# Kernel optimization log

Hardware: AMD Instinct MI355X
Metric: run time of the kernel (lower is better)

The kernel has to match this reference:

```python
import jax, jax.numpy as jnp
import numpy as np

S = 16        # neighbor samples per layer
NL = 2        # number of GNN layers


def setup_inputs() -> dict:
    key = jax.random.key(0)
    ks = jax.random.split(key, 12)
    N_NODES, D, E, NMP, DEG, N_EDGE, B, NC = 50000, 128, 32, 3, 32, 200000, 1024, 8
    sc = 0.05
    return {
        "ids": jax.random.randint(ks[0], (B,), 0, N_NODES, dtype=jnp.int32),
        "feats": jax.random.normal(ks[1], (N_NODES, D), jnp.float32),
        "edge_emb": jax.random.normal(ks[2], (NMP, N_EDGE, E), jnp.float32),
        "adj_nodes": jax.random.randint(ks[3], (NMP, N_NODES, DEG), 0, N_NODES, dtype=jnp.int32),
        "adj_edges": jax.random.randint(ks[4], (NMP, N_NODES, DEG), 0, N_EDGE, dtype=jnp.int32),
        "W_self": jax.random.normal(ks[5], (NMP, NL, D, D), jnp.float32) * sc,
        "W_neigh": jax.random.normal(ks[6], (NMP, NL, D + E, D), jnp.float32) * sc,
        "W_edge": jax.random.normal(ks[7], (NMP, NL, 2 * D + E, E), jnp.float32) * sc,
        "attn": jax.random.normal(ks[8], (D,), jnp.float32) * sc,
        "fc_w": jax.random.normal(ks[9], (D, NC), jnp.float32) * sc,
        "fc_b": jnp.zeros((NC,), jnp.float32),
    }


def reference(ids, feats, edge_emb, adj_nodes, adj_edges, W_self, W_neigh, W_edge, attn, fc_w, fc_b):
    NMP = adj_nodes.shape[0]
    outs = []
    for mp in range(NMP):
        # --- sample neighbor tree (deterministic: first S columns) ---
        cur = ids
        all_feats = [feats[cur]]
        all_edges = []
        for _ in range(NL):
            nb = adj_nodes[mp][cur][:, :S].reshape(-1)     # [N*S]
            eid = adj_edges[mp][cur][:, :S].reshape(-1)    # [N*S]
            all_edges.append(edge_emb[mp][eid])            # [N*S, E]
            cur = nb
            all_feats.append(feats[cur])
        # --- per-layer aggregation + edge update ---
        for l in range(NL):
            new_feats = []
            for k in range(len(all_feats) - 1):
                xs, xn, ee = all_feats[k], all_feats[k + 1], all_edges[k]
                N = xs.shape[0]
                # mean over sampled neighbors of [neigh_feat || edge_emb]
                nin = jnp.concatenate(
                    [xn.reshape(N, S, -1), ee.reshape(N, S, -1)], axis=-1
                ).mean(axis=1)                             # [N, D+E]
                new_feats.append(jax.nn.relu(xs @ W_self[mp, l] + nin @ W_neigh[mp, l]))
            all_feats = new_feats  # dropout is identity in eval mode
            new_edges = []
            for k in range(len(all_edges) - 1):
                xs, xn, ee = all_feats[k], all_feats[k + 1], all_edges[k]
                rep = jnp.repeat(xs, S, axis=0)            # [N*S, D]
                new_edges.append(jax.nn.relu(
                    jnp.concatenate([rep, xn, ee], axis=-1) @ W_edge[mp, l]))
            all_edges = new_edges
        outs.append(all_feats[0])                          # [B, D]
    stacked = jnp.stack(outs)                              # [NMP, B, D]
    # metapath attention fuse
    scores = jnp.tanh(jnp.einsum('mbd,d->mb', stacked, attn))
    beta = jax.nn.softmax(scores, axis=0)
    emb = jnp.einsum('mb,mbd->bd', beta, stacked)          # [B, D]
    # F.normalize(dim=1)
    emb = emb / jnp.maximum(jnp.linalg.norm(emb, axis=1, keepdims=True), 1e-12)
    return emb @ fc_w + fc_b
```

## Files before the change

kernel.cpp:

```cpp
#include <hip/hip_runtime.h>

#define NNODES  50000
#define D       128
#define E       32
#define NMP     3
#define DEG     32
#define NEDGE   200000
#define B       1024
#define NC      8
#define S       16

#define RPM      17408
#define NKT      9
#define WSTRIDE  36864
#define WESTRIDE 9216

#define CONV_TASKS (1600000 + 6 * WSTRIDE + 3 * WESTRIDE)
#define TOT_TASKS  (CONV_TASKS + 3 * RPM)

typedef float f4 __attribute__((ext_vector_type(4)));
typedef short bh8 __attribute__((ext_vector_type(8)));
typedef unsigned int uv4 __attribute__((ext_vector_type(4)));
typedef unsigned int uv2 __attribute__((ext_vector_type(2)));
typedef int iv4 __attribute__((ext_vector_type(4)));
typedef int iv2 __attribute__((ext_vector_type(2)));

static __device__ __forceinline__ unsigned short f2bf(float f) {
    unsigned int u = __float_as_uint(f);
    u = u + 0x7FFFu + ((u >> 16) & 1u);
    return (unsigned short)(u >> 16);
}
static __device__ __forceinline__ float bf2f(unsigned short h) {
    return __uint_as_float(((unsigned int)h) << 16);
}

__global__ __launch_bounds__(256) void convsamp_k(
    const float* __restrict__ feats, const float* __restrict__ Ws,
    const float* __restrict__ Wn, const float* __restrict__ We,
    const int* __restrict__ ids, const int* __restrict__ adjn,
    const int* __restrict__ adje,
    unsigned short* __restrict__ fb, unsigned short* __restrict__ WT0,
    unsigned short* __restrict__ WTe, int* __restrict__ gx, int* __restrict__ eid1)
{
    int i = blockIdx.x * 256 + threadIdx.x;
    if (i < 1600000) {
        float4 v = ((const float4*)feats)[i];
        unsigned int p0 = (unsigned int)f2bf(v.x) | ((unsigned int)f2bf(v.y) << 16);
        unsigned int p1 = (unsigned int)f2bf(v.z) | ((unsigned int)f2bf(v.w) << 16);
        ((uint2*)fb)[i] = make_uint2(p0, p1);
    } else if (i < 1600000 + 6 * WSTRIDE) {
        int i2 = i - 1600000;
        int ml = i2 / WSTRIDE, e = i2 % WSTRIDE;
        int j = e & 7, t1 = e >> 3;
        int n = t1 & 127, t2 = t1 >> 7;
        int q = t2 & 3, kt = t2 >> 2;
        int k = kt * 32 + q * 8 + j;
        float v = (k < 128) ? Ws[((size_t)ml * 128 + k) * 128 + n]
                            : Wn[((size_t)ml * 160 + (k - 128)) * 128 + n];
        WT0[(size_t)ml * WSTRIDE + e] = f2bf(v);
    } else if (i < CONV_TASKS) {
        int i3 = i - 1600000 - 6 * WSTRIDE;
        int mp = i3 / WESTRIDE, e = i3 % WESTRIDE;
        int j = e & 7, t1 = e >> 3;
        int n = t1 & 31, t2 = t1 >> 5;
        int q = t2 & 3, kt = t2 >> 2;
        int k = kt * 32 + q * 8 + j;
        float v = We[(((size_t)mp * 2) * 288 + k) * 32 + n];
        WTe[(size_t)mp * WESTRIDE + e] = f2bf(v);
    } else if (i < TOT_TASKS) {
        int i4 = i - CONV_TASKS;
        int mp = i4 / RPM, r = i4 % RPM;
        if (r < 16384) {
            int node = ids[r >> 4];
            gx[mp * RPM + r]     = adjn[((size_t)mp * NNODES + node) * DEG + (r & 15)];
            eid1[mp * 16384 + r] = adje[((size_t)mp * NNODES + node) * DEG + (r & 15)];
        } else {
            gx[mp * RPM + r] = ids[r - 16384];
        }
    }
}

__global__ __launch_bounds__(256, 3) void aggfeat_k(
    const unsigned short* __restrict__ fb, const float* __restrict__ edge_emb,
    const int* __restrict__ adjn, const int* __restrict__ adje,
    const int* __restrict__ gx, const int* __restrict__ eid1,
    const unsigned short* __restrict__ WT0,
    unsigned short* __restrict__ fout)
{
    __shared__ unsigned short Asm[16][136];
    __shared__ unsigned short Nsm[16][168];
    const int mp = blockIdx.y;
    const int w = threadIdx.x >> 6, l = threadIdx.x & 63;
    const int r0 = blockIdx.x * 16;
    const unsigned int* fb32 = (const unsigned int*)fb;
    const float* ee = edge_emb + (size_t)mp * NEDGE * E;
    const float inv = 1.0f / (float)S;
    const int g = l >> 4, c = l & 15;
    const int d8 = l & 7;

    iv4 srcv = *(const iv4*)(gx + mp * RPM + r0 + w * 4);

    iv4 nIdx[4]; iv2 eIdx[4]; unsigned int selfu[4];
#pragma unroll
    for (int rr = 0; rr < 4; ++rr) {
        const int src = srcv[rr];
        nIdx[rr]  = *(const iv4*)(adjn + ((size_t)mp * NNODES + src) * DEG + 4 * g);
        eIdx[rr]  = *(const iv2*)(adje + ((size_t)mp * NNODES + src) * DEG + 2 * (l >> 3));
        selfu[rr] = fb32[(size_t)src * 64 + l];
    }

    uv4 gN[4][4];
    f4  gE[4][2];
#pragma unroll
    for (int rr = 0; rr < 4; ++rr) {
#pragma unroll
        for (int p = 0; p < 4; ++p)
            gN[rr][p] = *(const uv4*)(fb32 + (size_t)nIdx[rr][p] * 64 + c * 4);
        gE[rr][0] = *(const f4*)(ee + (size_t)eIdx[rr][0] * E + d8 * 4);
        gE[rr][1] = *(const f4*)(ee + (size_t)eIdx[rr][1] * E + d8 * 4);
    }
    asm volatile("" ::: "memory");

#pragma unroll
    for (int rr = 0; rr < 4; ++rr) {
        const int lr = w * 4 + rr;
        float acc[8];
#pragma unroll
        for (int d = 0; d < 8; ++d) acc[d] = 0.f;
#pragma unroll
        for (int p = 0; p < 4; ++p)
#pragma unroll
            for (int qq = 0; qq < 4; ++qq) {
                unsigned int u = gN[rr][p][qq];
                acc[2 * qq]     += __uint_as_float(u << 16);
                acc[2 * qq + 1] += __uint_as_float(u & 0xffff0000u);
            }
#pragma unroll
        for (int d = 0; d < 8; ++d) {
            acc[d] += __shfl_xor(acc[d], 16);
            acc[d] += __shfl_xor(acc[d], 32);
        }
        float fe[4];
#pragma unroll
        for (int qq = 0; qq < 4; ++qq) {
            fe[qq] = gE[rr][0][qq] + gE[rr][1][qq];
            fe[qq] += __shfl_xor(fe[qq], 8);
            fe[qq] += __shfl_xor(fe[qq], 16);
            fe[qq] += __shfl_xor(fe[qq], 32);
        }

        ((unsigned int*)&Asm[lr][0])[l] = selfu[rr];
        if (g == 0) {
            uv4 o;
#pragma unroll
            for (int qq = 0; qq < 4; ++qq)
                o[qq] = (unsigned int)f2bf(acc[2 * qq] * inv)
                      | ((unsigned int)f2bf(acc[2 * qq + 1] * inv) << 16);
            *(uv4*)&Nsm[lr][c * 8] = o;
        }
        if (l < 8) {
            uv2 o;
            o[0] = (unsigned int)f2bf(fe[0] * inv) | ((unsigned int)f2bf(fe[1] * inv) << 16);
            o[1] = (unsigned int)f2bf(fe[2] * inv) | ((unsigned int)f2bf(fe[3] * inv) << 16);
            *(uv2*)&Nsm[lr][128 + d8 * 4] = o;
        }
    }
    __syncthreads();

    const int q = l >> 4, lm = l & 15;
    const unsigned short* wb = WT0 + (size_t)mp * 2 * WSTRIDE;

    f4 acc[2];
    acc[0] = (f4){0.f, 0.f, 0.f, 0.f};
    acc[1] = (f4){0.f, 0.f, 0.f, 0.f};

#pragma unroll
    for (int kt = 0; kt < NKT; ++kt) {
        const int k0 = kt * 32 + q * 8;
        bh8 a = (k0 < 128) ? *(const bh8*)&Asm[lm][k0]
                           : *(const bh8*)&Nsm[lm][k0 - 128];
        const unsigned short* wrow = wb + ((size_t)(kt * 4 + q) * 128 + lm) * 8;
#pragma unroll
        for (int ntl = 0; ntl < 2; ++ntl) {
            bh8 bf = *(const bh8*)(wrow + (w * 2 + ntl) * 16 * 8);
            acc[ntl] = __builtin_amdgcn_mfma_f32_16x16x32_bf16(a, bf, acc[ntl], 0, 0, 0);
        }
    }

#pragma unroll
    for (int ntl = 0; ntl < 2; ++ntl)
#pragma unroll
        for (int rr = 0; rr < 4; ++rr) {
            int row = r0 + q * 4 + rr;
            int col = (w * 2 + ntl) * 16 + lm;
            fout[((size_t)mp * RPM + row) * 128 + col] = f2bf(fmaxf(acc[ntl][rr], 0.f));
        }
}

__global__ __launch_bounds__(256) void edgeaggfin_k(
    const unsigned short* __restrict__ fout, const float* __restrict__ edge_emb,
    const int* __restrict__ eid1, const unsigned short* __restrict__ WTe,
    const unsigned short* __restrict__ WT0,
    const float* __restrict__ attn, const float* __restrict__ fcw,
    const float* __restrict__ fcb, float* __restrict__ out)
{
    __shared__ unsigned short As2[4][304];
    __shared__ float fembs[NMP][4][128];
    const int w = threadIdx.x >> 6, l = threadIdx.x & 63;
    const int q = l >> 4, lm = l & 15;
    const float inv = 1.0f / (float)S;

    for (int mp = 0; mp < NMP; ++mp) {
        const int m0 = (blockIdx.x * 4 + w) * 16;
        const unsigned short* we = WTe + (size_t)mp * WESTRIDE;
        const unsigned short* f1base = fout + (size_t)mp * RPM * 128;
        const unsigned short* f0base = fout + ((size_t)mp * RPM + 16384) * 128;
        const float* ee = edge_emb + (size_t)mp * NEDGE * E;

        const int row = m0 + lm;
        const unsigned short* a1p = f1base + (size_t)row * 128;
        const unsigned short* a0p = f0base + (size_t)(row >> 4) * 128;
        const int eidL = eid1[mp * 16384 + row];

        f4 acc[2];
        acc[0] = (f4){0.f, 0.f, 0.f, 0.f};
        acc[1] = (f4){0.f, 0.f, 0.f, 0.f};

#pragma unroll
        for (int kt = 0; kt < NKT; ++kt) {
            const int k0 = kt * 32 + q * 8;
            bh8 a;
            if (kt < 4) {
                a = *(const bh8*)(a0p + k0);
            } else if (kt < 8) {
                a = *(const bh8*)(a1p + (k0 - 128));
            } else {
                const float* ep = ee + (size_t)eidL * E + q * 8;
                float4 v0 = *(const float4*)ep;
                float4 v1 = *(const float4*)(ep + 4);
                bh8 tv;
                tv[0] = (short)f2bf(v0.x); tv[1] = (short)f2bf(v0.y);
                tv[2] = (short)f2bf(v0.z); tv[3] = (short)f2bf(v0.w);
                tv[4] = (short)f2bf(v1.x); tv[5] = (short)f2bf(v1.y);
                tv[6] = (short)f2bf(v1.z); tv[7] = (short)f2bf(v1.w);
                a = tv;
            }
            const unsigned short* wrow = we + ((size_t)(kt * 4 + q) * 32 + lm) * 8;
            bh8 b0 = *(const bh8*)(wrow);
            bh8 b1 = *(const bh8*)(wrow + 16 * 8);
            acc[0] = __builtin_amdgcn_mfma_f32_16x16x32_bf16(a, b0, acc[0], 0, 0, 0);
            acc[1] = __builtin_amdgcn_mfma_f32_16x16x32_bf16(a, b1, acc[1], 0, 0, 0);
        }

#pragma unroll
        for (int nt = 0; nt < 2; ++nt) {
            float ps = 0.f;
#pragma unroll
            for (int rr = 0; rr < 4; ++rr) ps += fmaxf(acc[nt][rr], 0.f);
            ps += __shfl_xor(ps, 16);
            ps += __shfl_xor(ps, 32);
            if (l < 16)
                As2[w][256 + nt * 16 + lm] = f2bf(ps * inv);
        }

        {
            const int seg = m0 >> 4;
            unsigned int f0u = ((const unsigned int*)a0p)[l];
            ((unsigned int*)&As2[w][0])[l] = f0u;

            const unsigned short* fr = f1base + (size_t)seg * 16 * 128;
            float s0 = 0.f, s1 = 0.f;
#pragma unroll
            for (int j = 0; j < S; ++j) {
                unsigned int u = ((const unsigned int*)(fr + j * 128))[l];
                s0 += bf2f((unsigned short)(u & 0xFFFF));
                s1 += bf2f((unsigned short)(u >> 16));
            }
            ((unsigned int*)&As2[w][0])[64 + l] =
                (unsigned int)f2bf(s0 * inv) | ((unsigned int)f2bf(s1 * inv) << 16);
        }
        __syncthreads();

        const unsigned short* wb1 = WT0 + ((size_t)mp * 2 + 1) * WSTRIDE;
        f4 acc2[2];
        acc2[0] = (f4){0.f, 0.f, 0.f, 0.f};
        acc2[1] = (f4){0.f, 0.f, 0.f, 0.f};

#pragma unroll
        for (int kt = 0; kt < NKT; ++kt) {
            const int k0 = kt * 32 + q * 8;
            bh8 a;
            if (lm < 4) a = *(const bh8*)&As2[lm][k0];
            else        a = (bh8){0, 0, 0, 0, 0, 0, 0, 0};
            const unsigned short* wrow = wb1 + ((size_t)(kt * 4 + q) * 128 + lm) * 8;
#pragma unroll
            for (int ntl = 0; ntl < 2; ++ntl) {
                bh8 bf = *(const bh8*)(wrow + (w * 2 + ntl) * 16 * 8);
                acc2[ntl] = __builtin_amdgcn_mfma_f32_16x16x32_bf16(a, bf, acc2[ntl], 0, 0, 0);
            }
        }
        if (q == 0) {
#pragma unroll
            for (int ntl = 0; ntl < 2; ++ntl)
#pragma unroll
                for (int rr = 0; rr < 4; ++rr)
                    fembs[mp][rr][(w * 2 + ntl) * 16 + lm] = fmaxf(acc2[ntl][rr], 0.f);
        }
        __syncthreads();
    }

    if (threadIdx.x < 32) {
        const int row = threadIdx.x >> 3;
        const int j = threadIdx.x & 7;
        const int d0 = j * 16;

        float sc[NMP];
#pragma unroll
        for (int mp = 0; mp < NMP; ++mp) {
            float p = 0.f;
#pragma unroll
            for (int d = 0; d < 16; ++d) p += fembs[mp][row][d0 + d] * attn[d0 + d];
            p += __shfl_xor(p, 1); p += __shfl_xor(p, 2); p += __shfl_xor(p, 4);
            sc[mp] = tanhf(p);
        }
        float mx = fmaxf(sc[0], fmaxf(sc[1], sc[2]));
        float e0 = expf(sc[0] - mx), e1 = expf(sc[1] - mx), e2 = expf(sc[2] - mx);
        float isum = 1.f / (e0 + e1 + e2);
        float b0 = e0 * isum, b1 = e1 * isum, b2 = e2 * isum;

        float emb[16];
        float nn = 0.f;
#pragma unroll
        for (int d = 0; d < 16; ++d) {
            float vv = b0 * fembs[0][row][d0 + d] + b1 * fembs[1][row][d0 + d]
                     + b2 * fembs[2][row][d0 + d];
            emb[d] = vv;
            nn += vv * vv;
        }
        nn += __shfl_xor(nn, 1); nn += __shfl_xor(nn, 2); nn += __shfl_xor(nn, 4);
        float innorm = 1.f / fmaxf(sqrtf(nn), 1e-12f);
#pragma unroll
        for (int d = 0; d < 16; ++d) emb[d] *= innorm;

        const int grow = blockIdx.x * 4 + row;
#pragma unroll
        for (int cc = 0; cc < NC; ++cc) {
            float p = 0.f;
#pragma unroll
            for (int d = 0; d < 16; ++d) p += emb[d] * fcw[(d0 + d) * NC + cc];
            p += __shfl_xor(p, 1); p += __shfl_xor(p, 2); p += __shfl_xor(p, 4);
            if (j == cc) out[(size_t)grow * NC + cc] = p + fcb[cc];
        }
    }
}

extern "C" void kernel_launch(void* const* d_in, const int* in_sizes, int n_in,
                              void* d_out, int out_size, void* d_ws, size_t ws_size,
                              hipStream_t stream) {
    const int* ids        = (const int*)d_in[0];
    const float* feats    = (const float*)d_in[1];
    const float* edge_emb = (const float*)d_in[2];
    const int* adjn       = (const int*)d_in[3];
    const int* adje       = (const int*)d_in[4];
    const float* Ws       = (const float*)d_in[5];
    const float* Wn       = (const float*)d_in[6];
    const float* We       = (const float*)d_in[7];
    const float* attn     = (const float*)d_in[8];
    const float* fcw      = (const float*)d_in[9];
    const float* fcb      = (const float*)d_in[10];
    float* out = (float*)d_out;

    char* p = (char*)d_ws;
    unsigned short* WT0 = (unsigned short*)p; p += (size_t)6 * WSTRIDE * 2;
    unsigned short* WTe = (unsigned short*)p; p += (size_t)3 * WESTRIDE * 2;
    unsigned short* fb  = (unsigned short*)p; p += (size_t)NNODES * 128 * 2;
    int* gx   = (int*)p;                      p += (size_t)3 * RPM * 4;
    int* eid1 = (int*)p;                      p += (size_t)3 * 16384 * 4;
    unsigned short* fout = (unsigned short*)p; p += (size_t)3 * RPM * 128 * 2;

    convsamp_k<<<TOT_TASKS / 256, 256, 0, stream>>>(feats, Ws, Wn, We, ids, adjn, adje,
                                                    fb, WT0, WTe, gx, eid1);
    aggfeat_k<<<dim3(RPM / 16, 3), 256, 0, stream>>>(fb, edge_emb, adjn, adje, gx, eid1,
                                                     WT0, fout);
    edgeaggfin_k<<<256, 256, 0, stream>>>(fout, edge_emb, eid1, WTe, WT0,
                                          attn, fcw, fcb, out);
}
```

Baseline: 225.9 us.

## Fuse three kernels into one persistent cooperative kernel with grid syncs

Replaces the three separate launches (conversion/sampling, feature aggregation, edge aggregation plus final fuse) with a single cooperative kernel of 768 persistent blocks that loops over the work and separates the phases with grid.sync. The aim is to remove launch gaps and tail effects between kernels. The final attention, normalize and fc step now runs in its own phase on only 32 blocks, with a new femb buffer holding per-metapath embeddings. The old three-kernel path stays as a fallback if the cooperative launch fails. In exchange it pays for grid-wide barriers and fixes occupancy at 3 blocks per CU.

```diff
diff --git a/kernel.cpp b/kernel.cpp
--- a/kernel.cpp
+++ b/kernel.cpp
@@ -1,4 +1,7 @@
 #include <hip/hip_runtime.h>
+#include <hip/hip_cooperative_groups.h>
+
+namespace cg = cooperative_groups;
 
 #define NNODES  50000
 #define D       128
@@ -14,6 +17,8 @@
 #define NKT      9
 #define WSTRIDE  36864
 #define WESTRIDE 9216
+#define NTILE    1088
+#define GRID     768
 
 #define CONV_TASKS (1600000 + 6 * WSTRIDE + 3 * WESTRIDE)
 #define TOT_TASKS  (CONV_TASKS + 3 * RPM)
@@ -32,6 +37,330 @@
 }
 static __device__ __forceinline__ float bf2f(unsigned short h) {
     return __uint_as_float(((unsigned int)h) << 16);
+}
+
+__global__ __launch_bounds__(256, 3) void fused_k(
+    const float* __restrict__ feats, const float* __restrict__ Ws,
+    const float* __restrict__ Wn, const float* __restrict__ We,
+    const int* __restrict__ ids, const int* __restrict__ adjn,
+    const int* __restrict__ adje, const float* __restrict__ edge_emb,
+    const float* __restrict__ attn, const float* __restrict__ fcw,
+    const float* __restrict__ fcb,
+    unsigned short* __restrict__ fb, unsigned short* __restrict__ WT0,
+    unsigned short* __restrict__ WTe, int* __restrict__ gx,
+    int* __restrict__ eid1, unsigned short* __restrict__ fout,
+    float* __restrict__ femb, float* __restrict__ out)
+{
+    cg::grid_group grid = cg::this_grid();
+    const int bid = blockIdx.x;
+    const int tid = threadIdx.x;
+    const int w = tid >> 6, l = tid & 63;
+    const float inv = 1.0f / (float)S;
+
+    __shared__ unsigned short Asm[16][136];
+    __shared__ unsigned short Nsm[16][168];
+    __shared__ unsigned short As2[4][304];
+
+    for (int i = bid * 256 + tid; i < TOT_TASKS; i += GRID * 256) {
+        if (i < 1600000) {
+            float4 v = ((const float4*)feats)[i];
+            unsigned int p0 = (unsigned int)f2bf(v.x) | ((unsigned int)f2bf(v.y) << 16);
+            unsigned int p1 = (unsigned int)f2bf(v.z) | ((unsigned int)f2bf(v.w) << 16);
+            ((uint2*)fb)[i] = make_uint2(p0, p1);
+        } else if (i < 1600000 + 6 * WSTRIDE) {
+            int i2 = i - 1600000;
+            int ml = i2 / WSTRIDE, e = i2 % WSTRIDE;
+            int j = e & 7, t1 = e >> 3;
+            int n = t1 & 127, t2 = t1 >> 7;
+            int q = t2 & 3, kt = t2 >> 2;
+            int k = kt * 32 + q * 8 + j;
+            float v = (k < 128) ? Ws[((size_t)ml * 128 + k) * 128 + n]
+                                : Wn[((size_t)ml * 160 + (k - 128)) * 128 + n];
+            WT0[(size_t)ml * WSTRIDE + e] = f2bf(v);
+        } else if (i < CONV_TASKS) {
+            int i3 = i - 1600000 - 6 * WSTRIDE;
+            int mp = i3 / WESTRIDE, e = i3 % WESTRIDE;
+            int j = e & 7, t1 = e >> 3;
+            int n = t1 & 31, t2 = t1 >> 5;
+            int q = t2 & 3, kt = t2 >> 2;
+            int k = kt * 32 + q * 8 + j;
+            float v = We[(((size_t)mp * 2) * 288 + k) * 32 + n];
+            WTe[(size_t)mp * WESTRIDE + e] = f2bf(v);
+        } else {
+            int i4 = i - CONV_TASKS;
+            int mp = i4 / RPM, r = i4 % RPM;
+            if (r < 16384) {
+                int node = ids[r >> 4];
+                gx[mp * RPM + r]     = adjn[((size_t)mp * NNODES + node) * DEG + (r & 15)];
+                eid1[mp * 16384 + r] = adje[((size_t)mp * NNODES + node) * DEG + (r & 15)];
+            } else {
+                gx[mp * RPM + r] = ids[r - 16384];
+            }
+        }
+    }
+    grid.sync();
+
+    {
+        const int g = l >> 4, c = l & 15;
+        const int d8 = l & 7;
+        const unsigned int* fb32 = (const unsigned int*)fb;
+        const int q = l >> 4, lm = l & 15;
+
+        for (int t = bid; t < NMP * NTILE; t += GRID) {
+            const int mp = t / NTILE, bx = t - mp * NTILE;
+            const int r0 = bx * 16;
+            const float* ee = edge_emb + (size_t)mp * NEDGE * E;
+
+            iv4 srcv = *(const iv4*)(gx + mp * RPM + r0 + w * 4);
+
+            iv4 nIdx[4]; iv2 eIdx[4]; unsigned int selfu[4];
+#pragma unroll
+            for (int rr = 0; rr < 4; ++rr) {
+                const int src = srcv[rr];
+                nIdx[rr]  = *(const iv4*)(adjn + ((size_t)mp * NNODES + src) * DEG + 4 * g);
+                eIdx[rr]  = *(const iv2*)(adje + ((size_t)mp * NNODES + src) * DEG + 2 * (l >> 3));
+                selfu[rr] = fb32[(size_t)src * 64 + l];
+            }
+
+            uv4 gN[4][4];
+            f4  gE[4][2];
+#pragma unroll
+            for (int rr = 0; rr < 4; ++rr) {
+#pragma unroll
+                for (int p = 0; p < 4; ++p)
+                    gN[rr][p] = *(const uv4*)(fb32 + (size_t)nIdx[rr][p] * 64 + c * 4);
+                gE[rr][0] = *(const f4*)(ee + (size_t)eIdx[rr][0] * E + d8 * 4);
+                gE[rr][1] = *(const f4*)(ee + (size_t)eIdx[rr][1] * E + d8 * 4);
+            }
+            asm volatile("" ::: "memory");
+
+#pragma unroll
+            for (int rr = 0; rr < 4; ++rr) {
+                const int lr = w * 4 + rr;
+                float acc[8];
+#pragma unroll
+                for (int d = 0; d < 8; ++d) acc[d] = 0.f;
+#pragma unroll
+                for (int p = 0; p < 4; ++p)
+#pragma unroll
+                    for (int qq = 0; qq < 4; ++qq) {
+                        unsigned int u = gN[rr][p][qq];
+                        acc[2 * qq]     += __uint_as_float(u << 16);
+                        acc[2 * qq + 1] += __uint_as_float(u & 0xffff0000u);
+                    }
+#pragma unroll
+                for (int d = 0; d < 8; ++d) {
+                    acc[d] += __shfl_xor(acc[d], 16);
+                    acc[d] += __shfl_xor(acc[d], 32);
+                }
+                float fe[4];
+#pragma unroll
+                for (int qq = 0; qq < 4; ++qq) {
+                    fe[qq] = gE[rr][0][qq] + gE[rr][1][qq];
+                    fe[qq] += __shfl_xor(fe[qq], 8);
+                    fe[qq] += __shfl_xor(fe[qq], 16);
+                    fe[qq] += __shfl_xor(fe[qq], 32);
+                }
+
+                ((unsigned int*)&Asm[lr][0])[l] = selfu[rr];
+                if (g == 0) {
+                    uv4 o;
+#pragma unroll
+                    for (int qq = 0; qq < 4; ++qq)
+                        o[qq] = (unsigned int)f2bf(acc[2 * qq] * inv)
+                              | ((unsigned int)f2bf(acc[2 * qq + 1] * inv) << 16);
+                    *(uv4*)&Nsm[lr][c * 8] = o;
+                }
+                if (l < 8) {
+                    uv2 o;
+                    o[0] = (unsigned int)f2bf(fe[0] * inv) | ((unsigned int)f2bf(fe[1] * inv) << 16);
+                    o[1] = (unsigned int)f2bf(fe[2] * inv) | ((unsigned int)f2bf(fe[3] * inv) << 16);
+                    *(uv2*)&Nsm[lr][128 + d8 * 4] = o;
+                }
+            }
+            __syncthreads();
+
+            const unsigned short* wb = WT0 + (size_t)mp * 2 * WSTRIDE;
+            f4 acc[2];
+            acc[0] = (f4){0.f, 0.f, 0.f, 0.f};
+            acc[1] = (f4){0.f, 0.f, 0.f, 0.f};
+#pragma unroll
+            for (int kt = 0; kt < NKT; ++kt) {
+                const int k0 = kt * 32 + q * 8;
+                bh8 a = (k0 < 128) ? *(const bh8*)&Asm[lm][k0]
+                                   : *(const bh8*)&Nsm[lm][k0 - 128];
+                const unsigned short* wrow = wb + ((size_t)(kt * 4 + q) * 128 + lm) * 8;
+#pragma unroll
+                for (int ntl = 0; ntl < 2; ++ntl) {
+                    bh8 bf = *(const bh8*)(wrow + (w * 2 + ntl) * 16 * 8);
+                    acc[ntl] = __builtin_amdgcn_mfma_f32_16x16x32_bf16(a, bf, acc[ntl], 0, 0, 0);
+                }
+            }
+#pragma unroll
+            for (int ntl = 0; ntl < 2; ++ntl)
+#pragma unroll
+                for (int rr = 0; rr < 4; ++rr) {
+                    int row = r0 + q * 4 + rr;
+                    int col = (w * 2 + ntl) * 16 + lm;
+                    fout[((size_t)mp * RPM + row) * 128 + col] = f2bf(fmaxf(acc[ntl][rr], 0.f));
+                }
+            __syncthreads();
+        }
+    }
+    grid.sync();
+
+    {
+        const int q = l >> 4, lm = l & 15;
+        const int mp = bid >> 8, sgrp = bid & 255;
+        const int m0 = sgrp * 64 + w * 16;
+        const unsigned short* we = WTe + (size_t)mp * WESTRIDE;
+        const unsigned short* f1base = fout + (size_t)mp * RPM * 128;
+        const unsigned short* f0base = fout + ((size_t)mp * RPM + 16384) * 128;
+        const float* ee = edge_emb + (size_t)mp * NEDGE * E;
+
+        const int row = m0 + lm;
+        const unsigned short* a1p = f1base + (size_t)row * 128;
+        const unsigned short* a0p = f0base + (size_t)(row >> 4) * 128;
+        const int eidL = eid1[mp * 16384 + row];
+
+        f4 acc[2];
+        acc[0] = (f4){0.f, 0.f, 0.f, 0.f};
+        acc[1] = (f4){0.f, 0.f, 0.f, 0.f};
+
+#pragma unroll
+        for (int kt = 0; kt < NKT; ++kt) {
+            const int k0 = kt * 32 + q * 8;
+            bh8 a;
+            if (kt < 4) {
+                a = *(const bh8*)(a0p + k0);
+            } else if (kt < 8) {
+                a = *(const bh8*)(a1p + (k0 - 128));
+            } else {
+                const float* ep = ee + (size_t)eidL * E + q * 8;
+                float4 v0 = *(const float4*)ep;
+                float4 v1 = *(const float4*)(ep + 4);
+                bh8 tv;
+                tv[0] = (short)f2bf(v0.x); tv[1] = (short)f2bf(v0.y);
+                tv[2] = (short)f2bf(v0.z); tv[3] = (short)f2bf(v0.w);
+                tv[4] = (short)f2bf(v1.x); tv[5] = (short)f2bf(v1.y);
+                tv[6] = (short)f2bf(v1.z); tv[7] = (short)f2bf(v1.w);
+                a = tv;
+            }
+            const unsigned short* wrow = we + ((size_t)(kt * 4 + q) * 32 + lm) * 8;
+            bh8 b0 = *(const bh8*)(wrow);
+            bh8 b1 = *(const bh8*)(wrow + 16 * 8);
+            acc[0] = __builtin_amdgcn_mfma_f32_16x16x32_bf16(a, b0, acc[0], 0, 0, 0);
+            acc[1] = __builtin_amdgcn_mfma_f32_16x16x32_bf16(a, b1, acc[1], 0, 0, 0);
+        }
+
+#pragma unroll
+        for (int nt = 0; nt < 2; ++nt) {
+            float ps = 0.f;
+#pragma unroll
+            for (int rr = 0; rr < 4; ++rr) ps += fmaxf(acc[nt][rr], 0.f);
+            ps += __shfl_xor(ps, 16);
+            ps += __shfl_xor(ps, 32);
+            if (l < 16)
+                As2[w][256 + nt * 16 + lm] = f2bf(ps * inv);
+        }
+
+        {
+            const int seg = m0 >> 4;
+            unsigned int f0u = ((const unsigned int*)a0p)[l];
+            ((unsigned int*)&As2[w][0])[l] = f0u;
+
+            const unsigned short* fr = f1base + (size_t)seg * 16 * 128;
+            float s0 = 0.f, s1 = 0.f;
+#pragma unroll
+            for (int j = 0; j < S; ++j) {
+                unsigned int u = ((const unsigned int*)(fr + j * 128))[l];
+                s0 += bf2f((unsigned short)(u & 0xFFFF));
+                s1 += bf2f((unsigned short)(u >> 16));
+            }
+            ((unsigned int*)&As2[w][0])[64 + l] =
+                (unsigned int)f2bf(s0 * inv) | ((unsigned int)f2bf(s1 * inv) << 16);
+        }
+        __syncthreads();
+
+        const unsigned short* wb1 = WT0 + ((size_t)mp * 2 + 1) * WSTRIDE;
+        f4 acc2[2];
+        acc2[0] = (f4){0.f, 0.f, 0.f, 0.f};
+        acc2[1] = (f4){0.f, 0.f, 0.f, 0.f};
+#pragma unroll
+        for (int kt = 0; kt < NKT; ++kt) {
+            const int k0 = kt * 32 + q * 8;
+            bh8 a;
+            if (lm < 4) a = *(const bh8*)&As2[lm][k0];
+            else        a = (bh8){0, 0, 0, 0, 0, 0, 0, 0};
+            const unsigned short* wrow = wb1 + ((size_t)(kt * 4 + q) * 128 + lm) * 8;
+#pragma unroll
+            for (int ntl = 0; ntl < 2; ++ntl) {
+                bh8 bf = *(const bh8*)(wrow + (w * 2 + ntl) * 16 * 8);
+                acc2[ntl] = __builtin_amdgcn_mfma_f32_16x16x32_bf16(a, bf, acc2[ntl], 0, 0, 0);
+            }
+        }
+        if (q == 0) {
+#pragma unroll
+            for (int ntl = 0; ntl < 2; ++ntl)
+#pragma unroll
+                for (int rr = 0; rr < 4; ++rr) {
+                    int seg = sgrp * 4 + rr;
+                    femb[((size_t)mp * B + seg) * 128 + (w * 2 + ntl) * 16 + lm] =
+                        fmaxf(acc2[ntl][rr], 0.f);
+                }
+        }
+    }
+    grid.sync();
+
+    if (bid < 32) {
+        const int row = bid * 32 + (tid >> 3);
+        const int j = tid & 7;
+        const int d0 = j * 16;
+
+        float v[NMP][16];
+#pragma unroll
+        for (int mp = 0; mp < NMP; ++mp)
+#pragma unroll
+            for (int t = 0; t < 4; ++t)
+                *(f4*)&v[mp][t * 4] =
+                    *(const f4*)&femb[((size_t)mp * B + row) * 128 + d0 + t * 4];
+
+        float sc[NMP];
+#pragma unroll
+        for (int mp = 0; mp < NMP; ++mp) {
+            float p = 0.f;
+#pragma unroll
+            for (int d = 0; d < 16; ++d) p += v[mp][d] * attn[d0 + d];
+            p += __shfl_xor(p, 1); p += __shfl_xor(p, 2); p += __shfl_xor(p, 4);
+            sc[mp] = tanhf(p);
+        }
+        float mx = fmaxf(sc[0], fmaxf(sc[1], sc[2]));
+        float e0 = expf(sc[0] - mx), e1 = expf(sc[1] - mx), e2 = expf(sc[2] - mx);
+        float isum = 1.f / (e0 + e1 + e2);
+        float b0 = e0 * isum, b1 = e1 * isum, b2 = e2 * isum;
+
+        float emb[16];
+        float nn = 0.f;
+#pragma unroll
+        for (int d = 0; d < 16; ++d) {
+            float vv = b0 * v[0][d] + b1 * v[1][d] + b2 * v[2][d];
+            emb[d] = vv;
+            nn += vv * vv;
+        }
+        nn += __shfl_xor(nn, 1); nn += __shfl_xor(nn, 2); nn += __shfl_xor(nn, 4);
+        float innorm = 1.f / fmaxf(sqrtf(nn), 1e-12f);
+#pragma unroll
+        for (int d = 0; d < 16; ++d) emb[d] *= innorm;
+
+#pragma unroll
+        for (int cc = 0; cc < NC; ++cc) {
+            float p = 0.f;
+#pragma unroll
+            for (int d = 0; d < 16; ++d) p += emb[d] * fcw[(d0 + d) * NC + cc];
+            p += __shfl_xor(p, 1); p += __shfl_xor(p, 2); p += __shfl_xor(p, 4);
+            if (j == cc) out[(size_t)row * NC + cc] = p + fcb[cc];
+        }
+    }
 }
 
 __global__ __launch_bounds__(256) void convsamp_k(
@@ -377,11 +706,24 @@
     int* gx   = (int*)p;                      p += (size_t)3 * RPM * 4;
     int* eid1 = (int*)p;                      p += (size_t)3 * 16384 * 4;
     unsigned short* fout = (unsigned short*)p; p += (size_t)3 * RPM * 128 * 2;
-
-    convsamp_k<<<TOT_TASKS / 256, 256, 0, stream>>>(feats, Ws, Wn, We, ids, adjn, adje,
-                                                    fb, WT0, WTe, gx, eid1);
-    aggfeat_k<<<dim3(RPM / 16, 3), 256, 0, stream>>>(fb, edge_emb, adjn, adje, gx, eid1,
-                                                     WT0, fout);
-    edgeaggfin_k<<<256, 256, 0, stream>>>(fout, edge_emb, eid1, WTe, WT0,
-                                          attn, fcw, fcb, out);
+    float* femb = (float*)p;                   p += (size_t)3 * B * 128 * 4;
+
+    void* args[] = {
+        (void*)&feats, (void*)&Ws, (void*)&Wn, (void*)&We,
+        (void*)&ids, (void*)&adjn, (void*)&adje, (void*)&edge_emb,
+        (void*)&attn, (void*)&fcw, (void*)&fcb,
+        (void*)&fb, (void*)&WT0, (void*)&WTe, (void*)&gx, (void*)&eid1,
+        (void*)&fout, (void*)&femb, (void*)&out
+    };
+    hipError_t err = hipLaunchCooperativeKernel(
+        (const void*)fused_k, dim3(GRID), dim3(256), args, 0, stream);
+    if (err != hipSuccess) {
+        (void)hipGetLastError();
+        convsamp_k<<<TOT_TASKS / 256, 256, 0, stream>>>(feats, Ws, Wn, We, ids, adjn,
+                                                        adje, fb, WT0, WTe, gx, eid1);
+        aggfeat_k<<<dim3(NTILE, 3), 256, 0, stream>>>(fb, edge_emb, adjn, adje, gx,
+                                                      eid1, WT0, fout);
+        edgeaggfin_k<<<256, 256, 0, stream>>>(fout, edge_emb, eid1, WTe, WT0,
+                                              attn, fcw, fcb, out);
+    }
 }
```

Result: slower. 496.8 us (+119.9%).
